# Optimization experiments

Hardware: AMD Instinct MI355X
Metric: run time of the kernel (lower is better)

## Reference

```python
import jax, jax.numpy as jnp
import numpy as np
from jax import lax

B, T = 128, 1024
RNN_DIM, EMB_DIM, ATT_DIM = 1024, 512, 128
N_FILT, KSIZE = 32, 31
PAD = KSIZE // 2  # 15


def setup_inputs() -> dict:
    key = jax.random.key(0)
    ks = jax.random.split(key, 8)
    return {
        "attention_hidden_state": jax.random.normal(ks[0], (B, RNN_DIM), jnp.float32),
        "memory": jax.random.normal(ks[1], (B, T, EMB_DIM), jnp.float32),
        "processed_memory": jax.random.normal(ks[2], (B, T, ATT_DIM), jnp.float32),
        "attention_weights_cat": jax.random.uniform(ks[3], (B, 2, T), jnp.float32),
        "mask": jnp.zeros((B, T), dtype=bool),
        # learned params
        "w_query": jax.random.normal(ks[4], (RNN_DIM, ATT_DIM), jnp.float32) * 0.02,
        "w_conv": jax.random.normal(ks[5], (N_FILT, 2, KSIZE), jnp.float32) * 0.1,   # OIH
        "w_loc": jax.random.normal(ks[6], (N_FILT, ATT_DIM), jnp.float32) * 0.1,
        "v": jax.random.normal(ks[7], (ATT_DIM,), jnp.float32) * 0.1,
    }


def reference(attention_hidden_state, memory, processed_memory,
              attention_weights_cat, mask, w_query, w_conv, w_loc, v):
    # processed_query: [B, 1, A] (broadcast over T)
    pq = (attention_hidden_state @ w_query)[:, None, :]
    # location features: Conv1d(2 -> N_FILT, pad=K//2, no bias) then Linear(N_FILT -> A)
    conv = lax.conv_general_dilated(
        attention_weights_cat, w_conv, window_strides=(1,),
        padding=[(PAD, PAD)], dimension_numbers=("NCH", "OIH", "NCH"))  # [B, F, T]
    loc = jnp.einsum("bft,fa->bta", conv, w_loc)  # [B, T, A]
    # energies: v^T tanh(pq + loc + pmem)  -> [B, T]
    energies = jnp.tanh(pq + loc + processed_memory) @ v
    energies = jnp.where(mask, -jnp.inf, energies)
    attention_weights = jax.nn.softmax(energies, axis=1)  # [B, T]
    attention_context = jnp.einsum("bt,btd->bd", attention_weights, memory)
    return attention_context, attention_weights
```

## Files before the change

### kernel.cpp

```cpp
#include <hip/hip_runtime.h>
#include <math.h>

#define BB    128
#define TT    1024
#define RNN   1024
#define EMBD  512
#define ATTD  128
#define NFILT 32
#define KSZ   31
#define PADK  15
#define CK    62
#define SPLIT 16
#define ETILE 128

__device__ __forceinline__ float fast_tanhf(float x) {
  const float ax = fabsf(x);
  const float t  = __expf(-2.f * ax);
  const float r  = (1.f - t) / (1.f + t);
  return copysignf(r, x);
}

__global__ __launch_bounds__(256) void k_pq_wl(const float* __restrict__ hid,
                                               const float* __restrict__ wq,
                                               const float* __restrict__ wconv,
                                               const float* __restrict__ wloc,
                                               float* __restrict__ pq,
                                               float* __restrict__ wl) {
  const int tid = threadIdx.x;
  if (blockIdx.x < BB) {
    const int b  = blockIdx.x;
    const int a  = tid & (ATTD - 1);
    const int kh = tid >> 7;
    __shared__ float sh[RNN];
    __shared__ float sred[ATTD];
    for (int i = tid; i < RNN; i += 256) sh[i] = hid[(size_t)b * RNN + i];
    __syncthreads();
    float acc = 0.f;
    const int k0 = kh * (RNN / 2);
    #pragma unroll 8
    for (int k = 0; k < RNN / 2; ++k)
      acc = fmaf(sh[k0 + k], wq[(size_t)(k0 + k) * ATTD + a], acc);
    if (kh == 1) sred[a] = acc;
    __syncthreads();
    if (kh == 0) pq[(size_t)b * ATTD + a] = acc + sred[a];
  } else {
    const int idx = (blockIdx.x - BB) * 256 + tid;
    const int ck = idx >> 7;
    const int a  = idx & (ATTD - 1);
    float acc = 0.f;
    #pragma unroll
    for (int f = 0; f < NFILT; ++f)
      acc = fmaf(wconv[f * CK + ck], wloc[f * ATTD + a], acc);
    wl[idx] = acc;
  }
}

__global__ __launch_bounds__(256) void k_energy(
    const float* __restrict__ awc,
    const float* __restrict__ pmem,
    const float* __restrict__ wl,
    const float* __restrict__ vvec,
    const float* __restrict__ pq,
    const unsigned char* __restrict__ mask,
    float* __restrict__ en)
{
  const int b  = blockIdx.x;
  const int t0 = blockIdx.y * ETILE;
  const int tid = threadIdx.x;
  __shared__ float s_aw[2][ETILE + 30];
  for (int i = tid; i < 2 * (ETILE + 30); i += 256) {
    const int c = (i < ETILE + 30) ? 0 : 1;
    const int j = c ? (i - (ETILE + 30)) : i;
    const int tg = t0 - PADK + j;
    s_aw[c][j] = (tg >= 0 && tg < TT) ? awc[((size_t)b * 2 + c) * TT + tg] : 0.f;
  }
  __syncthreads();

  const int lane = tid & 63;
  const int wave = tid >> 6;
  float2 wlr[CK];
  const float2* wl2 = (const float2*)wl;
  #pragma unroll
  for (int ck = 0; ck < CK; ++ck) wlr[ck] = wl2[ck * 64 + lane];
  const float2 pq2 = ((const float2*)(pq + (size_t)b * ATTD))[lane];
  const float2 v2  = ((const float2*)vvec)[lane];
  const float2* pm2 = (const float2*)(pmem + (size_t)b * TT * ATTD);

  const int tbase = wave * (ETILE / 4);
  float2 pm_next = pm2[(size_t)(t0 + tbase) * 64 + lane];
  #pragma unroll 2
  for (int i = 0; i < ETILE / 4; ++i) {
    const int tl = tbase + i;
    const int tg = t0 + tl;
    const float2 pm = pm_next;
    if (i + 1 < ETILE / 4)
      pm_next = pm2[(size_t)(tg + 1) * 64 + lane];
    float x0 = pq2.x + pm.x;
    float x1 = pq2.y + pm.y;
    #pragma unroll
    for (int k = 0; k < KSZ; ++k) {
      const float a0 = s_aw[0][tl + k];
      x0 = fmaf(a0, wlr[k].x, x0);
      x1 = fmaf(a0, wlr[k].y, x1);
    }
    #pragma unroll
    for (int k = 0; k < KSZ; ++k) {
      const float a1 = s_aw[1][tl + k];
      x0 = fmaf(a1, wlr[KSZ + k].x, x0);
      x1 = fmaf(a1, wlr[KSZ + k].y, x1);
    }
    float e = v2.x * fast_tanhf(x0) + v2.y * fast_tanhf(x1);
    #pragma unroll
    for (int off = 32; off; off >>= 1) e += __shfl_xor(e, off);
    if (lane == 0)
      en[(size_t)b * TT + tg] = mask[(size_t)b * TT + tg] ? -INFINITY : e;
  }
}

__global__ __launch_bounds__(256) void k_softmax(float* __restrict__ w) {
  const int b = blockIdx.x;
  const int tid = threadIdx.x;
  const int lane = tid & 63, wave = tid >> 6;
  __shared__ float red[8];
  float4* w4 = (float4*)(w + (size_t)b * TT);
  float4 e = w4[tid];
  float m = fmaxf(fmaxf(e.x, e.y), fmaxf(e.z, e.w));
  #pragma unroll
  for (int off = 32; off; off >>= 1) m = fmaxf(m, __shfl_xor(m, off));
  if (lane == 0) red[wave] = m;
  __syncthreads();
  m = fmaxf(fmaxf(red[0], red[1]), fmaxf(red[2], red[3]));
  float4 p;
  p.x = expf(e.x - m); p.y = expf(e.y - m);
  p.z = expf(e.z - m); p.w = expf(e.w - m);
  float s = p.x + p.y + p.z + p.w;
  #pragma unroll
  for (int off = 32; off; off >>= 1) s += __shfl_xor(s, off);
  if (lane == 0) red[4 + wave] = s;
  __syncthreads();
  const float inv = 1.f / (red[4] + red[5] + red[6] + red[7]);
  p.x *= inv; p.y *= inv; p.z *= inv; p.w *= inv;
  w4[tid] = p;
}

__global__ __launch_bounds__(128) void k_ctx_part(const float* __restrict__ wts,
                                                  const float* __restrict__ mem,
                                                  float* __restrict__ part) {
  const int b = blockIdx.x, s = blockIdx.y, tid = threadIdx.x;
  const float4* m4 = (const float4*)(mem + (size_t)b * TT * EMBD);
  const int tbeg = s * (TT / SPLIT);
  const float4* w4 = (const float4*)(wts + (size_t)b * TT + tbeg);
  float4 acc = make_float4(0.f, 0.f, 0.f, 0.f);
  for (int i4 = 0; i4 < TT / SPLIT / 4; ++i4) {
    const float4 wv = w4[i4];
    #pragma unroll 4
    for (int j = 0; j < 4; ++j) {
      const int t = tbeg + i4 * 4 + j;
      const float w = (j == 0) ? wv.x : (j == 1) ? wv.y : (j == 2) ? wv.z : wv.w;
      const float4 mv = m4[(size_t)t * (EMBD / 4) + tid];
      acc.x = fmaf(w, mv.x, acc.x);
      acc.y = fmaf(w, mv.y, acc.y);
      acc.z = fmaf(w, mv.z, acc.z);
      acc.w = fmaf(w, mv.w, acc.w);
    }
  }
  ((float4*)part)[((size_t)s * BB + b) * (EMBD / 4) + tid] = acc;
}

__global__ void k_ctx_reduce(const float* __restrict__ part,
                             float* __restrict__ ctx) {
  const int j = blockIdx.x * 256 + threadIdx.x;
  const float4* p4 = (const float4*)part;
  float4 acc = p4[j];
  #pragma unroll
  for (int s = 1; s < SPLIT; ++s) {
    const float4 v = p4[(size_t)s * (BB * EMBD / 4) + j];
    acc.x += v.x; acc.y += v.y; acc.z += v.z; acc.w += v.w;
  }
  ((float4*)ctx)[j] = acc;
}

extern "C" void kernel_launch(void* const* d_in, const int* in_sizes, int n_in,
                              void* d_out, int out_size, void* d_ws, size_t ws_size,
                              hipStream_t stream) {
  const float* hid   = (const float*)d_in[0];
  const float* mem   = (const float*)d_in[1];
  const float* pmem  = (const float*)d_in[2];
  const float* awc   = (const float*)d_in[3];
  const unsigned char* mask = (const unsigned char*)d_in[4];
  const float* wq    = (const float*)d_in[5];
  const float* wconv = (const float*)d_in[6];
  const float* wloc  = (const float*)d_in[7];
  const float* v     = (const float*)d_in[8];

  float* out = (float*)d_out;
  float* ctx = out;
  float* wts = out + BB * EMBD;

  char* ws = (char*)d_ws;
  float* pq   = (float*)(ws);
  float* wl   = (float*)(ws + 65536);
  float* part = (float*)(ws + (1 << 20));

  k_pq_wl<<<BB + 31, 256, 0, stream>>>(hid, wq, wconv, wloc, pq, wl);
  k_energy<<<dim3(BB, TT / ETILE), 256, 0, stream>>>(awc, pmem, wl, v, pq, mask, wts);
  k_softmax<<<BB, 256, 0, stream>>>(wts);
  k_ctx_part<<<dim3(BB, SPLIT), 128, 0, stream>>>(wts, mem, part);
  k_ctx_reduce<<<64, 256, 0, stream>>>(part, ctx);
}
```

Measured before the change: 509.6 us.

## Fuse energy, split softmax and context into one kernel with flash-style combine

Merges the energy, softmax and partial-context kernels into one kernel per (batch, T-chunk), computing local max/sum and unnormalized weights in shared memory. A combine kernel rescales the partial contexts and weights using the per-chunk maxima, as in online softmax. This removes a global round trip of energies and weights and two launches. In exchange the energy phase now runs with 128 threads per block without prefetching, and the occupancy hint of 3 blocks may limit registers for the 62 float2 weight registers.

```diff
diff --git a/kernel.cpp b/kernel.cpp
--- a/kernel.cpp
+++ b/kernel.cpp
@@ -11,7 +11,7 @@
 #define PADK  15
 #define CK    62
 #define SPLIT 16
-#define ETILE 128
+#define TSP   (TT / SPLIT)
 
 __device__ __forceinline__ float fast_tanhf(float x) {
   const float ax = fabsf(x);
@@ -55,29 +55,37 @@
   }
 }
 
-__global__ __launch_bounds__(256) void k_energy(
+__global__ __launch_bounds__(128, 3) void k_fused(
     const float* __restrict__ awc,
     const float* __restrict__ pmem,
+    const float* __restrict__ mem,
     const float* __restrict__ wl,
     const float* __restrict__ vvec,
     const float* __restrict__ pq,
     const unsigned char* __restrict__ mask,
-    float* __restrict__ en)
+    float* __restrict__ wts,
+    float* __restrict__ part_ctx,
+    float* __restrict__ part_ms,
+    float* __restrict__ part_sum)
 {
-  const int b  = blockIdx.x;
-  const int t0 = blockIdx.y * ETILE;
-  const int tid = threadIdx.x;
-  __shared__ float s_aw[2][ETILE + 30];
-  for (int i = tid; i < 2 * (ETILE + 30); i += 256) {
-    const int c = (i < ETILE + 30) ? 0 : 1;
-    const int j = c ? (i - (ETILE + 30)) : i;
+  const int blk  = blockIdx.x;
+  const int b    = blk & (BB - 1);
+  const int s    = blk >> 7;
+  const int tid  = threadIdx.x;
+  const int lane = tid & 63;
+  const int wave = tid >> 6;
+  const int t0   = s * TSP;
+
+  __shared__ float s_aw[2][TSP + 30];
+  __shared__ float s_p[TSP];
+
+  for (int i = tid; i < 2 * (TSP + 30); i += 128) {
+    const int c  = (i >= TSP + 30);
+    const int j  = c ? i - (TSP + 30) : i;
     const int tg = t0 - PADK + j;
     s_aw[c][j] = (tg >= 0 && tg < TT) ? awc[((size_t)b * 2 + c) * TT + tg] : 0.f;
   }
-  __syncthreads();
-
-  const int lane = tid & 63;
-  const int wave = tid >> 6;
+
   float2 wlr[CK];
   const float2* wl2 = (const float2*)wl;
   #pragma unroll
@@ -85,16 +93,12 @@
   const float2 pq2 = ((const float2*)(pq + (size_t)b * ATTD))[lane];
   const float2 v2  = ((const float2*)vvec)[lane];
   const float2* pm2 = (const float2*)(pmem + (size_t)b * TT * ATTD);
-
-  const int tbase = wave * (ETILE / 4);
-  float2 pm_next = pm2[(size_t)(t0 + tbase) * 64 + lane];
-  #pragma unroll 2
-  for (int i = 0; i < ETILE / 4; ++i) {
-    const int tl = tbase + i;
+  __syncthreads();
+
+  for (int i = 0; i < TSP / 2; ++i) {
+    const int tl = wave * (TSP / 2) + i;
     const int tg = t0 + tl;
-    const float2 pm = pm_next;
-    if (i + 1 < ETILE / 4)
-      pm_next = pm2[(size_t)(tg + 1) * 64 + lane];
+    const float2 pm = pm2[(size_t)tg * 64 + lane];
     float x0 = pq2.x + pm.x;
     float x1 = pq2.y + pm.y;
     #pragma unroll
@@ -112,72 +116,82 @@
     float e = v2.x * fast_tanhf(x0) + v2.y * fast_tanhf(x1);
     #pragma unroll
     for (int off = 32; off; off >>= 1) e += __shfl_xor(e, off);
-    if (lane == 0)
-      en[(size_t)b * TT + tg] = mask[(size_t)b * TT + tg] ? -INFINITY : e;
-  }
-}
-
-__global__ __launch_bounds__(256) void k_softmax(float* __restrict__ w) {
-  const int b = blockIdx.x;
+    if (lane == 0) s_p[tl] = e;
+  }
+  __syncthreads();
+
+  if (wave == 0) {
+    float e = s_p[lane];
+    if (mask[(size_t)b * TT + t0 + lane]) e = -INFINITY;
+    float m = e;
+    #pragma unroll
+    for (int off = 32; off; off >>= 1) m = fmaxf(m, __shfl_xor(m, off));
+    const float p = __expf(e - m);
+    float sum = p;
+    #pragma unroll
+    for (int off = 32; off; off >>= 1) sum += __shfl_xor(sum, off);
+    s_p[lane] = p;
+    wts[(size_t)b * TT + t0 + lane] = p;
+    if (lane == 0) {
+      part_ms [(size_t)s * BB + b] = m;
+      part_sum[(size_t)s * BB + b] = sum;
+    }
+  }
+  __syncthreads();
+
+  const float4* m4 = (const float4*)(mem + (size_t)b * TT * EMBD) + (size_t)t0 * (EMBD / 4);
+  float4 acc = make_float4(0.f, 0.f, 0.f, 0.f);
+  #pragma unroll 8
+  for (int t = 0; t < TSP; ++t) {
+    const float p  = s_p[t];
+    const float4 mv = m4[(size_t)t * (EMBD / 4) + tid];
+    acc.x = fmaf(p, mv.x, acc.x);
+    acc.y = fmaf(p, mv.y, acc.y);
+    acc.z = fmaf(p, mv.z, acc.z);
+    acc.w = fmaf(p, mv.w, acc.w);
+  }
+  ((float4*)part_ctx)[((size_t)s * BB + b) * (EMBD / 4) + tid] = acc;
+}
+
+__global__ __launch_bounds__(128) void k_combine(
+    const float* __restrict__ part_ctx,
+    const float* __restrict__ part_ms,
+    const float* __restrict__ part_sum,
+    float* __restrict__ ctx,
+    float* __restrict__ wts)
+{
+  const int b   = blockIdx.x;
   const int tid = threadIdx.x;
-  const int lane = tid & 63, wave = tid >> 6;
-  __shared__ float red[8];
-  float4* w4 = (float4*)(w + (size_t)b * TT);
-  float4 e = w4[tid];
-  float m = fmaxf(fmaxf(e.x, e.y), fmaxf(e.z, e.w));
-  #pragma unroll
-  for (int off = 32; off; off >>= 1) m = fmaxf(m, __shfl_xor(m, off));
-  if (lane == 0) red[wave] = m;
-  __syncthreads();
-  m = fmaxf(fmaxf(red[0], red[1]), fmaxf(red[2], red[3]));
-  float4 p;
-  p.x = expf(e.x - m); p.y = expf(e.y - m);
-  p.z = expf(e.z - m); p.w = expf(e.w - m);
-  float s = p.x + p.y + p.z + p.w;
-  #pragma unroll
-  for (int off = 32; off; off >>= 1) s += __shfl_xor(s, off);
-  if (lane == 0) red[4 + wave] = s;
-  __syncthreads();
-  const float inv = 1.f / (red[4] + red[5] + red[6] + red[7]);
-  p.x *= inv; p.y *= inv; p.z *= inv; p.w *= inv;
-  w4[tid] = p;
-}
-
-__global__ __launch_bounds__(128) void k_ctx_part(const float* __restrict__ wts,
-                                                  const float* __restrict__ mem,
-                                                  float* __restrict__ part) {
-  const int b = blockIdx.x, s = blockIdx.y, tid = threadIdx.x;
-  const float4* m4 = (const float4*)(mem + (size_t)b * TT * EMBD);
-  const int tbeg = s * (TT / SPLIT);
-  const float4* w4 = (const float4*)(wts + (size_t)b * TT + tbeg);
+  __shared__ float s_a[SPLIT];
+
+  float M = -INFINITY;
+  #pragma unroll
+  for (int s = 0; s < SPLIT; ++s) M = fmaxf(M, part_ms[(size_t)s * BB + b]);
+  float T = 0.f;
+  #pragma unroll
+  for (int s = 0; s < SPLIT; ++s)
+    T += part_sum[(size_t)s * BB + b] * __expf(part_ms[(size_t)s * BB + b] - M);
+  const float invT = 1.f / T;
+  if (tid < SPLIT) s_a[tid] = __expf(part_ms[(size_t)tid * BB + b] - M) * invT;
+  __syncthreads();
+
   float4 acc = make_float4(0.f, 0.f, 0.f, 0.f);
-  for (int i4 = 0; i4 < TT / SPLIT / 4; ++i4) {
-    const float4 wv = w4[i4];
-    #pragma unroll 4
-    for (int j = 0; j < 4; ++j) {
-      const int t = tbeg + i4 * 4 + j;
-      const float w = (j == 0) ? wv.x : (j == 1) ? wv.y : (j == 2) ? wv.z : wv.w;
-      const float4 mv = m4[(size_t)t * (EMBD / 4) + tid];
-      acc.x = fmaf(w, mv.x, acc.x);
-      acc.y = fmaf(w, mv.y, acc.y);
-      acc.z = fmaf(w, mv.z, acc.z);
-      acc.w = fmaf(w, mv.w, acc.w);
-    }
-  }
-  ((float4*)part)[((size_t)s * BB + b) * (EMBD / 4) + tid] = acc;
-}
-
-__global__ void k_ctx_reduce(const float* __restrict__ part,
-                             float* __restrict__ ctx) {
-  const int j = blockIdx.x * 256 + threadIdx.x;
-  const float4* p4 = (const float4*)part;
-  float4 acc = p4[j];
-  #pragma unroll
-  for (int s = 1; s < SPLIT; ++s) {
-    const float4 v = p4[(size_t)s * (BB * EMBD / 4) + j];
-    acc.x += v.x; acc.y += v.y; acc.z += v.z; acc.w += v.w;
-  }
-  ((float4*)ctx)[j] = acc;
+  #pragma unroll
+  for (int s = 0; s < SPLIT; ++s) {
+    const float a = s_a[s];
+    const float4 v = ((const float4*)part_ctx)[((size_t)s * BB + b) * (EMBD / 4) + tid];
+    acc.x = fmaf(a, v.x, acc.x);
+    acc.y = fmaf(a, v.y, acc.y);
+    acc.z = fmaf(a, v.z, acc.z);
+    acc.w = fmaf(a, v.w, acc.w);
+  }
+  ((float4*)ctx)[(size_t)b * (EMBD / 4) + tid] = acc;
+
+  #pragma unroll
+  for (int i = 0; i < TT / 128; ++i) {
+    const int t = i * 128 + tid;
+    wts[(size_t)b * TT + t] *= s_a[t >> 6];
+  }
 }
 
 extern "C" void kernel_launch(void* const* d_in, const int* in_sizes, int n_in,
@@ -198,13 +212,14 @@
   float* wts = out + BB * EMBD;
 
   char* ws = (char*)d_ws;
-  float* pq   = (float*)(ws);
-  float* wl   = (float*)(ws + 65536);
-  float* part = (float*)(ws + (1 << 20));
+  float* pq       = (float*)(ws);
+  float* wl       = (float*)(ws + (64 << 10));
+  float* part_ms  = (float*)(ws + (128 << 10));
+  float* part_sum = (float*)(ws + (192 << 10));
+  float* part_ctx = (float*)(ws + (1 << 20));
 
   k_pq_wl<<<BB + 31, 256, 0, stream>>>(hid, wq, wconv, wloc, pq, wl);
-  k_energy<<<dim3(BB, TT / ETILE), 256, 0, stream>>>(awc, pmem, wl, v, pq, mask, wts);
-  k_softmax<<<BB, 256, 0, stream>>>(wts);
-  k_ctx_part<<<dim3(BB, SPLIT), 128, 0, stream>>>(wts, mem, part);
-  k_ctx_reduce<<<64, 256, 0, stream>>>(part, ctx);
-}
+  k_fused<<<SPLIT * BB, 128, 0, stream>>>(awc, pmem, mem, wl, v, pq, mask,
+                                          wts, part_ctx, part_ms, part_sum);
+  k_combine<<<BB, 128, 0, stream>>>(part_ctx, part_ms, part_sum, ctx, wts);
+}
```

Result: faster. 498.7 us (-2.1%).
